# Kernel tuning notes

Measured on AMD Instinct MI355X. Metric: run time of the kernel, lower is better.

The kernel has to match this reference:

```python
import jax, jax.numpy as jnp
import numpy as np

NUM_HEADS = 12
H_PATCH = 14
W_PATCH = 14
ROPE_BASE = 10000.0


def _rope_2d(head_dim):
    # 2D RoPE: first half of head_dim encodes row (h), second half encodes col (w).
    half = head_dim // 2
    inv_freq = 1.0 / (ROPE_BASE ** (jnp.arange(0, half, 2, dtype=jnp.float32) / half))  # [half/2]
    ys = jnp.arange(H_PATCH)
    xs = jnp.arange(W_PATCH)
    yy, xx = jnp.meshgrid(ys, xs, indexing='ij')
    h_idx = yy.reshape(-1).astype(jnp.float32)  # [N]
    w_idx = xx.reshape(-1).astype(jnp.float32)  # [N]
    freqs_h = h_idx[:, None] * inv_freq[None, :]  # [N, half/2]
    freqs_w = w_idx[:, None] * inv_freq[None, :]  # [N, half/2]
    emb = jnp.concatenate([freqs_h, freqs_w], axis=-1)  # [N, half]
    emb = jnp.concatenate([emb, emb], axis=-1)          # [N, head_dim]
    return jnp.cos(emb), jnp.sin(emb)


def _rotate_half(x):
    d = x.shape[-1] // 2
    return jnp.concatenate([-x[..., d:], x[..., :d]], axis=-1)


def reference(x, qkv_w, qkv_b, proj_w, proj_b):
    BxT, N, C = x.shape
    hd = C // NUM_HEADS
    qkv = x @ qkv_w.T + qkv_b                                    # [BxT, N, 3C]
    qkv = qkv.reshape(BxT, N, 3, NUM_HEADS, hd)
    qkv = jnp.transpose(qkv, (2, 0, 3, 1, 4))                    # [3, BxT, H, N, hd]
    q, k, v = qkv[0], qkv[1], qkv[2]
    cos, sin = _rope_2d(hd)                                      # [N, hd]
    cos = cos[None, None, :, :]
    sin = sin[None, None, :, :]
    q = q * cos + _rotate_half(q) * sin
    k = k * cos + _rotate_half(k) * sin
    scale = hd ** -0.5
    attn = jnp.einsum('bhqd,bhkd->bhqk', q, k) * scale           # [BxT, H, N, N]
    attn = jax.nn.softmax(attn, axis=-1)
    out = jnp.einsum('bhqk,bhkd->bhqd', attn, v)                 # [BxT, H, N, hd]
    out = jnp.transpose(out, (0, 2, 1, 3)).reshape(BxT, N, C)
    out = out @ proj_w.T + proj_b
    return out


def setup_inputs() -> dict:
    key = jax.random.key(0)
    ks = jax.random.split(key, 5)
    C = 768
    return {
        'x': jax.random.normal(ks[0], (128, 196, C), dtype=jnp.float32),
        'qkv_w': jax.random.normal(ks[1], (3 * C, C), dtype=jnp.float32) * (C ** -0.5),
        'qkv_b': jax.random.normal(ks[2], (3 * C,), dtype=jnp.float32) * 0.02,
        'proj_w': jax.random.normal(ks[3], (C, C), dtype=jnp.float32) * (C ** -0.5),
        'proj_b': jax.random.normal(ks[4], (C,), dtype=jnp.float32) * 0.02,
    }
```

## Files before the change

### kernel.cpp

```cpp
#include <hip/hip_runtime.h>
#include <hip/hip_bf16.h>

typedef __attribute__((ext_vector_type(8))) short short8;
typedef __attribute__((ext_vector_type(4))) float f32x4;

#define GLD16(gp, lp) \
  __builtin_amdgcn_global_load_lds((const __attribute__((address_space(1))) void*)(gp), \
                                   (__attribute__((address_space(3))) void*)(lp), 16, 0, 0)

__device__ __forceinline__ f32x4 mfma_bf16(short8 a, short8 b, f32x4 c) {
  return __builtin_amdgcn_mfma_f32_16x16x32_bf16(a, b, c, 0, 0, 0);
}

__global__ __launch_bounds__(256) void cast_bf16_kernel(const float* __restrict__ src,
                                                        __hip_bfloat16* __restrict__ dst,
                                                        int n4) {
  int i = blockIdx.x * 256 + threadIdx.x;
  if (i >= n4) return;
  float4 v = reinterpret_cast<const float4*>(src)[i];
  ushort4 o;
  o.x = __builtin_bit_cast(unsigned short, __float2bfloat16(v.x));
  o.y = __builtin_bit_cast(unsigned short, __float2bfloat16(v.y));
  o.z = __builtin_bit_cast(unsigned short, __float2bfloat16(v.z));
  o.w = __builtin_bit_cast(unsigned short, __float2bfloat16(v.w));
  reinterpret_cast<ushort4*>(dst)[i] = o;
}

__global__ __launch_bounds__(256) void rope_table_kernel(float* __restrict__ cosT,
                                                         float* __restrict__ sinT) {
  int i = blockIdx.x * 256 + threadIdx.x;
  if (i >= 196 * 64) return;
  int t = i >> 6, d = i & 63;
  int c = d & 31;
  float pos = (c < 16) ? (float)(t / 14) : (float)(t % 14);
  int j = c & 15;
  float invf = expf(-(float)j * 0.5756462732485114f);
  float ang = pos * invf;
  cosT[i] = cosf(ang);
  sinT[i] = sinf(ang);
}

__global__ __launch_bounds__(256) void gemm_qkv_kernel(
    const __hip_bfloat16* __restrict__ A, const __hip_bfloat16* __restrict__ W,
    const float* __restrict__ bias, const float* __restrict__ cosT,
    const float* __restrict__ sinT, __hip_bfloat16* __restrict__ qb,
    __hip_bfloat16* __restrict__ kb, __hip_bfloat16* __restrict__ vb) {
  __shared__ __align__(16) __hip_bfloat16 As[128 * 64];
  __shared__ __align__(16) __hip_bfloat16 Bs[128 * 64];
  const int tid = threadIdx.x;
  const int id = blockIdx.x;
  const int sup = id / 72, rem = id % 72;
  const int bm = sup * 4 + rem / 18;
  const int bn = rem % 18;
  const int lane = tid & 63, wv = tid >> 6;
  const int wm = wv >> 1, wn = wv & 1;
  const int quad = lane >> 4, ln = lane & 15;

  const int r0 = tid >> 3;
  const int csw = ((tid & 7) ^ (r0 & 7)) * 8;
  const __hip_bfloat16* Ag = A + ((long)(bm * 128 + r0) * 768 + csw);
  const __hip_bfloat16* Wg = W + ((long)(bn * 128 + r0) * 768 + csw);
  __hip_bfloat16* As0 = As + tid * 8;
  __hip_bfloat16* Bs0 = Bs + tid * 8;

  const int c0 = (quad ^ (ln & 7)) * 8;
  const int c1 = c0 ^ 32;

  f32x4 acc[4][4];
#pragma unroll
  for (int i = 0; i < 4; i++)
#pragma unroll
    for (int j = 0; j < 4; j++) acc[i][j] = (f32x4){0.f, 0.f, 0.f, 0.f};

  for (int k0 = 0; k0 < 768; k0 += 64) {
    GLD16(Ag + k0,            As0);
    GLD16(Ag + 32 * 768 + k0, As0 + 2048);
    GLD16(Ag + 64 * 768 + k0, As0 + 4096);
    GLD16(Ag + 96 * 768 + k0, As0 + 6144);
    GLD16(Wg + k0,            Bs0);
    GLD16(Wg + 32 * 768 + k0, Bs0 + 2048);
    GLD16(Wg + 64 * 768 + k0, Bs0 + 4096);
    GLD16(Wg + 96 * 768 + k0, Bs0 + 6144);
    __syncthreads();
#pragma unroll
    for (int kk = 0; kk < 2; kk++) {
      const int cc = kk ? c1 : c0;
      short8 af[4], bf[4];
#pragma unroll
      for (int i = 0; i < 4; i++)
        af[i] = *(const short8*)(As + (wm * 64 + i * 16 + ln) * 64 + cc);
#pragma unroll
      for (int j = 0; j < 4; j++)
        bf[j] = *(const short8*)(Bs + (wn * 64 + j * 16 + ln) * 64 + cc);
#pragma unroll
      for (int i = 0; i < 4; i++)
#pragma unroll
        for (int j = 0; j < 4; j++) acc[i][j] = mfma_bf16(af[i], bf[j], acc[i][j]);
    }
    __syncthreads();
  }

  const int ncolbase = bn * 128 + wn * 64;
  const int s = ncolbase / 768;
  const int hh = (ncolbase % 768) >> 6;
  __hip_bfloat16* outb = (s == 0) ? qb : ((s == 1) ? kb : vb);
  float bi[4];
#pragma unroll
  for (int j = 0; j < 4; j++) bi[j] = bias[ncolbase + j * 16 + ln];
  const bool dorope = (s < 2);

#pragma unroll
  for (int i = 0; i < 4; i++) {
#pragma unroll
    for (int r = 0; r < 4; r++) {
      int m = bm * 128 + wm * 64 + i * 16 + quad * 4 + r;
      int b = m / 196, t = m - b * 196;
      float v0 = acc[i][0][r] + bi[0];
      float v1 = acc[i][1][r] + bi[1];
      float v2 = acc[i][2][r] + bi[2];
      float v3 = acc[i][3][r] + bi[3];
      if (dorope) {
        const float* ct = cosT + t * 64 + ln;
        const float* st = sinT + t * 64 + ln;
        float c0f = ct[0], c1f = ct[16], c2f = ct[32], c3f = ct[48];
        float s0 = st[0], s1 = st[16], s2 = st[32], s3 = st[48];
        float w0 = v0 * c0f - v2 * s0;
        float w1 = v1 * c1f - v3 * s1;
        float w2 = v2 * c2f + v0 * s2;
        float w3 = v3 * c3f + v1 * s3;
        v0 = w0; v1 = w1; v2 = w2; v3 = w3;
      }
      __hip_bfloat16* op = outb + ((long)(b * 12 + hh) * 196 + t) * 64 + ln;
      op[0]  = __float2bfloat16(v0);
      op[16] = __float2bfloat16(v1);
      op[32] = __float2bfloat16(v2);
      op[48] = __float2bfloat16(v3);
    }
  }
}

__global__ __launch_bounds__(256) void attn_kernel(
    const __hip_bfloat16* __restrict__ qb, const __hip_bfloat16* __restrict__ kb,
    const __hip_bfloat16* __restrict__ vb, __hip_bfloat16* __restrict__ att) {
  __shared__ __align__(16) __hip_bfloat16 Vt[64 * 232];
  __shared__ __align__(16) __hip_bfloat16 Ps[4][16 * 232];
  const int bh = blockIdx.x;
  const int b = bh / 12, h = bh - b * 12;
  const int tid = threadIdx.x;
  const int lane = tid & 63, wv = tid >> 6;
  const int quad = lane >> 4, ln = lane & 15;
  const __hip_bfloat16* qg = qb + (long)bh * (196 * 64);
  const __hip_bfloat16* kg = kb + (long)bh * (196 * 64);
  const __hip_bfloat16* vg = vb + (long)bh * (196 * 64);

  for (int ch = tid; ch < 224 * 8; ch += 256) {
    int row = ch >> 3, c = (ch & 7) * 8;
    unsigned short vals[8] = {0, 0, 0, 0, 0, 0, 0, 0};
    if (row < 196) *(uint4*)vals = *(const uint4*)(vg + row * 64 + c);
#pragma unroll
    for (int u = 0; u < 8; u++)
      ((unsigned short*)Vt)[(c + u) * 232 + row] = vals[u];
  }

  __hip_bfloat16* Pw = &Ps[wv][0];
#pragma unroll
  for (int r = 0; r < 4; r++)
    Pw[(quad * 4 + r) * 232 + 208 + ln] = __float2bfloat16(0.f);
  __syncthreads();

  for (int qt = wv; qt < 13; qt += 4) {
    int tok = qt * 16 + ln;
    if (tok > 195) tok = 195;
    short8 aq0 = *(const short8*)(qg + tok * 64 + quad * 8);
    short8 aq1 = *(const short8*)(qg + tok * 64 + 32 + quad * 8);

    f32x4 sacc[13];
#pragma unroll
    for (int ct = 0; ct < 13; ct++) {
      int krow = ct * 16 + ln;
      if (krow > 195) krow = 195;
      const __hip_bfloat16* kp = kg + krow * 64 + quad * 8;
      short8 b0 = *(const short8*)kp;
      short8 b1 = *(const short8*)(kp + 32);
      f32x4 cacc = (f32x4){0.f, 0.f, 0.f, 0.f};
      cacc = mfma_bf16(aq0, b0, cacc);
      cacc = mfma_bf16(aq1, b1, cacc);
      sacc[ct] = cacc;
    }

    float sm[4] = {0.f, 0.f, 0.f, 0.f};
#pragma unroll
    for (int ct = 0; ct < 13; ct++) {
      bool valid = (ct * 16 + ln) < 196;
#pragma unroll
      for (int r = 0; r < 4; r++) {
        float p = valid ? __expf(sacc[ct][r] * 0.125f) : 0.f;
        sm[r] += p;
        Pw[(quad * 4 + r) * 232 + ct * 16 + ln] = __float2bfloat16(p);
      }
    }
#pragma unroll
    for (int mk = 1; mk < 16; mk <<= 1) {
#pragma unroll
      for (int r = 0; r < 4; r++) sm[r] += __shfl_xor(sm[r], mk, 64);
    }
    asm volatile("" ::: "memory");

    f32x4 o[4];
#pragma unroll
    for (int j = 0; j < 4; j++) o[j] = (f32x4){0.f, 0.f, 0.f, 0.f};
#pragma unroll
    for (int kt = 0; kt < 7; kt++) {
      short8 pa = *(const short8*)(Pw + ln * 232 + kt * 32 + quad * 8);
#pragma unroll
      for (int j = 0; j < 4; j++) {
        short8 bv = *(const short8*)(Vt + (j * 16 + ln) * 232 + kt * 32 + quad * 8);
        o[j] = mfma_bf16(pa, bv, o[j]);
      }
    }
    asm volatile("" ::: "memory");

    float rl[4];
#pragma unroll
    for (int r = 0; r < 4; r++) rl[r] = 1.0f / sm[r];
    int trow = qt * 16 + quad * 4;
#pragma unroll
    for (int r = 0; r < 4; r++) {
      int t = trow + r;
      if (t < 196) {
        __hip_bfloat16* op = att + (long)(b * 196 + t) * 768 + h * 64 + ln;
#pragma unroll
        for (int j = 0; j < 4; j++) op[j * 16] = __float2bfloat16(o[j][r] * rl[r]);
      }
    }
  }
}

__global__ __launch_bounds__(256) void gemm_proj_kernel(
    const __hip_bfloat16* __restrict__ A, const __hip_bfloat16* __restrict__ W,
    const float* __restrict__ bias, float* __restrict__ out) {
  __shared__ __align__(16) __hip_bfloat16 As[128 * 64];
  __shared__ __align__(16) __hip_bfloat16 Bs[128 * 64];
  const int tid = threadIdx.x;
  const int id = blockIdx.x;
  const int sup = id / 24, rem = id % 24;
  const int bm = sup * 4 + rem / 6;
  const int bn = rem % 6;
  const int lane = tid & 63, wv = tid >> 6;
  const int wm = wv >> 1, wn = wv & 1;
  const int quad = lane >> 4, ln = lane & 15;

  const int r0 = tid >> 3;
  const int csw = ((tid & 7) ^ (r0 & 7)) * 8;
  const __hip_bfloat16* Ag = A + ((long)(bm * 128 + r0) * 768 + csw);
  const __hip_bfloat16* Wg = W + ((long)(bn * 128 + r0) * 768 + csw);
  __hip_bfloat16* As0 = As + tid * 8;
  __hip_bfloat16* Bs0 = Bs + tid * 8;

  const int c0 = (quad ^ (ln & 7)) * 8;
  const int c1 = c0 ^ 32;

  f32x4 acc[4][4];
#pragma unroll
  for (int i = 0; i < 4; i++)
#pragma unroll
    for (int j = 0; j < 4; j++) acc[i][j] = (f32x4){0.f, 0.f, 0.f, 0.f};

  for (int k0 = 0; k0 < 768; k0 += 64) {
    GLD16(Ag + k0,            As0);
    GLD16(Ag + 32 * 768 + k0, As0 + 2048);
    GLD16(Ag + 64 * 768 + k0, As0 + 4096);
    GLD16(Ag + 96 * 768 + k0, As0 + 6144);
    GLD16(Wg + k0,            Bs0);
    GLD16(Wg + 32 * 768 + k0, Bs0 + 2048);
    GLD16(Wg + 64 * 768 + k0, Bs0 + 4096);
    GLD16(Wg + 96 * 768 + k0, Bs0 + 6144);
    __syncthreads();
#pragma unroll
    for (int kk = 0; kk < 2; kk++) {
      const int cc = kk ? c1 : c0;
      short8 af[4], bf[4];
#pragma unroll
      for (int i = 0; i < 4; i++)
        af[i] = *(const short8*)(As + (wm * 64 + i * 16 + ln) * 64 + cc);
#pragma unroll
      for (int j = 0; j < 4; j++)
        bf[j] = *(const short8*)(Bs + (wn * 64 + j * 16 + ln) * 64 + cc);
#pragma unroll
      for (int i = 0; i < 4; i++)
#pragma unroll
        for (int j = 0; j < 4; j++) acc[i][j] = mfma_bf16(af[i], bf[j], acc[i][j]);
    }
    __syncthreads();
  }

  const int ncolbase = bn * 128 + wn * 64;
  float bi[4];
#pragma unroll
  for (int j = 0; j < 4; j++) bi[j] = bias[ncolbase + j * 16 + ln];
#pragma unroll
  for (int i = 0; i < 4; i++) {
#pragma unroll
    for (int r = 0; r < 4; r++) {
      int m = bm * 128 + wm * 64 + i * 16 + quad * 4 + r;
      float* op = out + (long)m * 768 + ncolbase + ln;
      op[0]  = acc[i][0][r] + bi[0];
      op[16] = acc[i][1][r] + bi[1];
      op[32] = acc[i][2][r] + bi[2];
      op[48] = acc[i][3][r] + bi[3];
    }
  }
}

extern "C" void kernel_launch(void* const* d_in, const int* in_sizes, int n_in,
                              void* d_out, int out_size, void* d_ws, size_t ws_size,
                              hipStream_t stream) {
  const float* x      = (const float*)d_in[0];
  const float* qkv_w  = (const float*)d_in[1];
  const float* qkv_b  = (const float*)d_in[2];
  const float* proj_w = (const float*)d_in[3];
  const float* proj_b = (const float*)d_in[4];
  float* out = (float*)d_out;
  (void)in_sizes; (void)n_in; (void)out_size; (void)ws_size;

  char* ws = (char*)d_ws;
  size_t off = 0;
  auto alloc = [&](size_t bytes) -> void* {
    void* p = (void*)(ws + off);
    off += (bytes + 255) & ~(size_t)255;
    return p;
  };
  const size_t MB0 = (size_t)25088 * 768 * 2;
  __hip_bfloat16* xb   = (__hip_bfloat16*)alloc(MB0);
  __hip_bfloat16* w1b  = (__hip_bfloat16*)alloc((size_t)2304 * 768 * 2);
  __hip_bfloat16* w2b  = (__hip_bfloat16*)alloc((size_t)768 * 768 * 2);
  float* cosT          = (float*)alloc(196 * 64 * 4);
  float* sinT          = (float*)alloc(196 * 64 * 4);
  __hip_bfloat16* qbuf = (__hip_bfloat16*)alloc(MB0);
  __hip_bfloat16* kbuf = (__hip_bfloat16*)alloc(MB0);
  __hip_bfloat16* vbuf = (__hip_bfloat16*)alloc(MB0);
  __hip_bfloat16* attb = xb;

  cast_bf16_kernel<<<18816, 256, 0, stream>>>(x, xb, 25088 * 768 / 4);
  cast_bf16_kernel<<<1728, 256, 0, stream>>>(qkv_w, w1b, 2304 * 768 / 4);
  cast_bf16_kernel<<<576, 256, 0, stream>>>(proj_w, w2b, 768 * 768 / 4);
  rope_table_kernel<<<49, 256, 0, stream>>>(cosT, sinT);
  gemm_qkv_kernel<<<3528, 256, 0, stream>>>(xb, w1b, qkv_b, cosT, sinT,
                                            qbuf, kbuf, vbuf);
  attn_kernel<<<1536, 256, 0, stream>>>(qbuf, kbuf, vbuf, attb);
  gemm_proj_kernel<<<1176, 256, 0, stream>>>(attb, w2b, proj_b, out);
}
```

Baseline: 378.0 us.

## Widen GEMM N-tiles to 256 and merge cast/rope prep into one kernel

Both GEMMs move from 128x128 to 128x256 block tiles, so each wave computes a 64x128 sub-tile with a 4x8 MFMA accumulator array. This halves the grid and raises reuse of A fragments per LDS load. It also drops the grouped (super-block) rasterization in favour of a plain row-major order. The three cast launches and the rope-table launch are folded into a single prep kernel to cut launch overhead. In exchange, the larger tiles double the accumulator registers and B-tile LDS, which lowers occupancy, and the proj GEMM now launches only 588 blocks.

```diff
diff --git a/kernel.cpp b/kernel.cpp
--- a/kernel.cpp
+++ b/kernel.cpp
@@ -12,32 +12,42 @@
   return __builtin_amdgcn_mfma_f32_16x16x32_bf16(a, b, c, 0, 0, 0);
 }
 
-__global__ __launch_bounds__(256) void cast_bf16_kernel(const float* __restrict__ src,
-                                                        __hip_bfloat16* __restrict__ dst,
-                                                        int n4) {
+__global__ __launch_bounds__(256) void prep_kernel(
+    const float* __restrict__ x, const float* __restrict__ w1,
+    const float* __restrict__ w2, __hip_bfloat16* __restrict__ xb,
+    __hip_bfloat16* __restrict__ w1b, __hip_bfloat16* __restrict__ w2b,
+    float* __restrict__ cosT, float* __restrict__ sinT) {
+  const int N1 = 4816896;
+  const int N2 = N1 + 442368;
+  const int N3 = N2 + 147456;
   int i = blockIdx.x * 256 + threadIdx.x;
-  if (i >= n4) return;
-  float4 v = reinterpret_cast<const float4*>(src)[i];
-  ushort4 o;
-  o.x = __builtin_bit_cast(unsigned short, __float2bfloat16(v.x));
-  o.y = __builtin_bit_cast(unsigned short, __float2bfloat16(v.y));
-  o.z = __builtin_bit_cast(unsigned short, __float2bfloat16(v.z));
-  o.w = __builtin_bit_cast(unsigned short, __float2bfloat16(v.w));
-  reinterpret_cast<ushort4*>(dst)[i] = o;
-}
-
-__global__ __launch_bounds__(256) void rope_table_kernel(float* __restrict__ cosT,
-                                                         float* __restrict__ sinT) {
-  int i = blockIdx.x * 256 + threadIdx.x;
-  if (i >= 196 * 64) return;
-  int t = i >> 6, d = i & 63;
-  int c = d & 31;
-  float pos = (c < 16) ? (float)(t / 14) : (float)(t % 14);
-  int j = c & 15;
-  float invf = expf(-(float)j * 0.5756462732485114f);
-  float ang = pos * invf;
-  cosT[i] = cosf(ang);
-  sinT[i] = sinf(ang);
+  if (i < N3) {
+    const float* src;
+    __hip_bfloat16* dst;
+    int j;
+    if (i < N1) { src = x; dst = xb; j = i; }
+    else if (i < N2) { src = w1; dst = w1b; j = i - N1; }
+    else { src = w2; dst = w2b; j = i - N2; }
+    float4 v = reinterpret_cast<const float4*>(src)[j];
+    ushort4 o;
+    o.x = __builtin_bit_cast(unsigned short, __float2bfloat16(v.x));
+    o.y = __builtin_bit_cast(unsigned short, __float2bfloat16(v.y));
+    o.z = __builtin_bit_cast(unsigned short, __float2bfloat16(v.z));
+    o.w = __builtin_bit_cast(unsigned short, __float2bfloat16(v.w));
+    reinterpret_cast<ushort4*>(dst)[j] = o;
+  } else {
+    int r = i - N3;
+    if (r < 196 * 64) {
+      int t = r >> 6, d = r & 63;
+      int c = d & 31;
+      float pos = (c < 16) ? (float)(t / 14) : (float)(t % 14);
+      int jj = c & 15;
+      float invf = expf(-(float)jj * 0.5756462732485114f);
+      float ang = pos * invf;
+      cosT[r] = cosf(ang);
+      sinT[r] = sinf(ang);
+    }
+  }
 }
 
 __global__ __launch_bounds__(256) void gemm_qkv_kernel(
@@ -46,12 +56,10 @@
     const float* __restrict__ sinT, __hip_bfloat16* __restrict__ qb,
     __hip_bfloat16* __restrict__ kb, __hip_bfloat16* __restrict__ vb) {
   __shared__ __align__(16) __hip_bfloat16 As[128 * 64];
-  __shared__ __align__(16) __hip_bfloat16 Bs[128 * 64];
+  __shared__ __align__(16) __hip_bfloat16 Bs[256 * 64];
   const int tid = threadIdx.x;
   const int id = blockIdx.x;
-  const int sup = id / 72, rem = id % 72;
-  const int bm = sup * 4 + rem / 18;
-  const int bn = rem % 18;
+  const int bm = id / 9, bn = id % 9;
   const int lane = tid & 63, wv = tid >> 6;
   const int wm = wv >> 1, wn = wv & 1;
   const int quad = lane >> 4, ln = lane & 15;
@@ -59,54 +67,50 @@
   const int r0 = tid >> 3;
   const int csw = ((tid & 7) ^ (r0 & 7)) * 8;
   const __hip_bfloat16* Ag = A + ((long)(bm * 128 + r0) * 768 + csw);
-  const __hip_bfloat16* Wg = W + ((long)(bn * 128 + r0) * 768 + csw);
+  const __hip_bfloat16* Wg = W + ((long)(bn * 256 + r0) * 768 + csw);
   __hip_bfloat16* As0 = As + tid * 8;
   __hip_bfloat16* Bs0 = Bs + tid * 8;
 
   const int c0 = (quad ^ (ln & 7)) * 8;
   const int c1 = c0 ^ 32;
 
-  f32x4 acc[4][4];
+  f32x4 acc[4][8];
 #pragma unroll
   for (int i = 0; i < 4; i++)
 #pragma unroll
-    for (int j = 0; j < 4; j++) acc[i][j] = (f32x4){0.f, 0.f, 0.f, 0.f};
+    for (int j = 0; j < 8; j++) acc[i][j] = (f32x4){0.f, 0.f, 0.f, 0.f};
 
   for (int k0 = 0; k0 < 768; k0 += 64) {
-    GLD16(Ag + k0,            As0);
-    GLD16(Ag + 32 * 768 + k0, As0 + 2048);
-    GLD16(Ag + 64 * 768 + k0, As0 + 4096);
-    GLD16(Ag + 96 * 768 + k0, As0 + 6144);
-    GLD16(Wg + k0,            Bs0);
-    GLD16(Wg + 32 * 768 + k0, Bs0 + 2048);
-    GLD16(Wg + 64 * 768 + k0, Bs0 + 4096);
-    GLD16(Wg + 96 * 768 + k0, Bs0 + 6144);
+#pragma unroll
+    for (int b = 0; b < 4; b++) GLD16(Ag + (long)b * 32 * 768 + k0, As0 + b * 2048);
+#pragma unroll
+    for (int b = 0; b < 8; b++) GLD16(Wg + (long)b * 32 * 768 + k0, Bs0 + b * 2048);
     __syncthreads();
 #pragma unroll
     for (int kk = 0; kk < 2; kk++) {
       const int cc = kk ? c1 : c0;
-      short8 af[4], bf[4];
+      short8 af[4], bf[8];
 #pragma unroll
       for (int i = 0; i < 4; i++)
         af[i] = *(const short8*)(As + (wm * 64 + i * 16 + ln) * 64 + cc);
 #pragma unroll
-      for (int j = 0; j < 4; j++)
-        bf[j] = *(const short8*)(Bs + (wn * 64 + j * 16 + ln) * 64 + cc);
+      for (int j = 0; j < 8; j++)
+        bf[j] = *(const short8*)(Bs + (wn * 128 + j * 16 + ln) * 64 + cc);
 #pragma unroll
       for (int i = 0; i < 4; i++)
 #pragma unroll
-        for (int j = 0; j < 4; j++) acc[i][j] = mfma_bf16(af[i], bf[j], acc[i][j]);
+        for (int j = 0; j < 8; j++) acc[i][j] = mfma_bf16(af[i], bf[j], acc[i][j]);
     }
     __syncthreads();
   }
 
-  const int ncolbase = bn * 128 + wn * 64;
-  const int s = ncolbase / 768;
-  const int hh = (ncolbase % 768) >> 6;
+  const int ncb = bn * 256 + wn * 128;
+  const int s = ncb / 768;
+  const int h0 = (ncb % 768) >> 6;
   __hip_bfloat16* outb = (s == 0) ? qb : ((s == 1) ? kb : vb);
-  float bi[4];
-#pragma unroll
-  for (int j = 0; j < 4; j++) bi[j] = bias[ncolbase + j * 16 + ln];
+  float bi[8];
+#pragma unroll
+  for (int j = 0; j < 8; j++) bi[j] = bias[ncb + j * 16 + ln];
   const bool dorope = (s < 2);
 
 #pragma unroll
@@ -115,26 +119,31 @@
     for (int r = 0; r < 4; r++) {
       int m = bm * 128 + wm * 64 + i * 16 + quad * 4 + r;
       int b = m / 196, t = m - b * 196;
-      float v0 = acc[i][0][r] + bi[0];
-      float v1 = acc[i][1][r] + bi[1];
-      float v2 = acc[i][2][r] + bi[2];
-      float v3 = acc[i][3][r] + bi[3];
+      float v[8];
+#pragma unroll
+      for (int j = 0; j < 8; j++) v[j] = acc[i][j][r] + bi[j];
       if (dorope) {
         const float* ct = cosT + t * 64 + ln;
         const float* st = sinT + t * 64 + ln;
-        float c0f = ct[0], c1f = ct[16], c2f = ct[32], c3f = ct[48];
-        float s0 = st[0], s1 = st[16], s2 = st[32], s3 = st[48];
-        float w0 = v0 * c0f - v2 * s0;
-        float w1 = v1 * c1f - v3 * s1;
-        float w2 = v2 * c2f + v0 * s2;
-        float w3 = v3 * c3f + v1 * s3;
-        v0 = w0; v1 = w1; v2 = w2; v3 = w3;
+        float cv[4], sv[4];
+#pragma unroll
+        for (int u = 0; u < 4; u++) { cv[u] = ct[u * 16]; sv[u] = st[u * 16]; }
+#pragma unroll
+        for (int p = 0; p < 4; p++) {
+          int jl = (p & 1) + (p & 2) * 2;
+          int jh = jl + 2;
+          int dl = jl & 3, dh = dl + 2;
+          float lo = v[jl] * cv[dl] - v[jh] * sv[dl];
+          float hi = v[jh] * cv[dh] + v[jl] * sv[dh];
+          v[jl] = lo; v[jh] = hi;
+        }
       }
-      __hip_bfloat16* op = outb + ((long)(b * 12 + hh) * 196 + t) * 64 + ln;
-      op[0]  = __float2bfloat16(v0);
-      op[16] = __float2bfloat16(v1);
-      op[32] = __float2bfloat16(v2);
-      op[48] = __float2bfloat16(v3);
+      __hip_bfloat16* op0 = outb + ((long)(b * 12 + h0) * 196 + t) * 64 + ln;
+      __hip_bfloat16* op1 = op0 + 196 * 64;
+#pragma unroll
+      for (int j = 0; j < 4; j++) op0[j * 16] = __float2bfloat16(v[j]);
+#pragma unroll
+      for (int j = 0; j < 4; j++) op1[j * 16] = __float2bfloat16(v[4 + j]);
     }
   }
 }
@@ -240,12 +249,10 @@
     const __hip_bfloat16* __restrict__ A, const __hip_bfloat16* __restrict__ W,
     const float* __restrict__ bias, float* __restrict__ out) {
   __shared__ __align__(16) __hip_bfloat16 As[128 * 64];
-  __shared__ __align__(16) __hip_bfloat16 Bs[128 * 64];
+  __shared__ __align__(16) __hip_bfloat16 Bs[256 * 64];
   const int tid = threadIdx.x;
   const int id = blockIdx.x;
-  const int sup = id / 24, rem = id % 24;
-  const int bm = sup * 4 + rem / 6;
-  const int bn = rem % 6;
+  const int bm = id / 3, bn = id % 3;
   const int lane = tid & 63, wv = tid >> 6;
   const int wm = wv >> 1, wn = wv & 1;
   const int quad = lane >> 4, ln = lane & 15;
@@ -253,61 +260,55 @@
   const int r0 = tid >> 3;
   const int csw = ((tid & 7) ^ (r0 & 7)) * 8;
   const __hip_bfloat16* Ag = A + ((long)(bm * 128 + r0) * 768 + csw);
-  const __hip_bfloat16* Wg = W + ((long)(bn * 128 + r0) * 768 + csw);
+  const __hip_bfloat16* Wg = W + ((long)(bn * 256 + r0) * 768 + csw);
   __hip_bfloat16* As0 = As + tid * 8;
   __hip_bfloat16* Bs0 = Bs + tid * 8;
 
   const int c0 = (quad ^ (ln & 7)) * 8;
   const int c1 = c0 ^ 32;
 
-  f32x4 acc[4][4];
+  f32x4 acc[4][8];
 #pragma unroll
   for (int i = 0; i < 4; i++)
 #pragma unroll
-    for (int j = 0; j < 4; j++) acc[i][j] = (f32x4){0.f, 0.f, 0.f, 0.f};
+    for (int j = 0; j < 8; j++) acc[i][j] = (f32x4){0.f, 0.f, 0.f, 0.f};
 
   for (int k0 = 0; k0 < 768; k0 += 64) {
-    GLD16(Ag + k0,            As0);
-    GLD16(Ag + 32 * 768 + k0, As0 + 2048);
-    GLD16(Ag + 64 * 768 + k0, As0 + 4096);
-    GLD16(Ag + 96 * 768 + k0, As0 + 6144);
-    GLD16(Wg + k0,            Bs0);
-    GLD16(Wg + 32 * 768 + k0, Bs0 + 2048);
-    GLD16(Wg + 64 * 768 + k0, Bs0 + 4096);
-    GLD16(Wg + 96 * 768 + k0, Bs0 + 6144);
+#pragma unroll
+    for (int b = 0; b < 4; b++) GLD16(Ag + (long)b * 32 * 768 + k0, As0 + b * 2048);
+#pragma unroll
+    for (int b = 0; b < 8; b++) GLD16(Wg + (long)b * 32 * 768 + k0, Bs0 + b * 2048);
     __syncthreads();
 #pragma unroll
     for (int kk = 0; kk < 2; kk++) {
       const int cc = kk ? c1 : c0;
-      short8 af[4], bf[4];
+      short8 af[4], bf[8];
 #pragma unroll
       for (int i = 0; i < 4; i++)
         af[i] = *(const short8*)(As + (wm * 64 + i * 16 + ln) * 64 + cc);
 #pragma unroll
-      for (int j = 0; j < 4; j++)
-        bf[j] = *(const short8*)(Bs + (wn * 64 + j * 16 + ln) * 64 + cc);
+      for (int j = 0; j < 8; j++)
+        bf[j] = *(const short8*)(Bs + (wn * 128 + j * 16 + ln) * 64 + cc);
 #pragma unroll
       for (int i = 0; i < 4; i++)
 #pragma unroll
-        for (int j = 0; j < 4; j++) acc[i][j] = mfma_bf16(af[i], bf[j], acc[i][j]);
+        for (int j = 0; j < 8; j++) acc[i][j] = mfma_bf16(af[i], bf[j], acc[i][j]);
     }
     __syncthreads();
   }
 
-  const int ncolbase = bn * 128 + wn * 64;
-  float bi[4];
-#pragma unroll
-  for (int j = 0; j < 4; j++) bi[j] = bias[ncolbase + j * 16 + ln];
+  const int ncb = bn * 256 + wn * 128;
+  float bi[8];
+#pragma unroll
+  for (int j = 0; j < 8; j++) bi[j] = bias[ncb + j * 16 + ln];
 #pragma unroll
   for (int i = 0; i < 4; i++) {
 #pragma unroll
     for (int r = 0; r < 4; r++) {
       int m = bm * 128 + wm * 64 + i * 16 + quad * 4 + r;
-      float* op = out + (long)m * 768 + ncolbase + ln;
-      op[0]  = acc[i][0][r] + bi[0];
-      op[16] = acc[i][1][r] + bi[1];
-      op[32] = acc[i][2][r] + bi[2];
-      op[48] = acc[i][3][r] + bi[3];
+      float* op = out + (long)m * 768 + ncb + ln;
+#pragma unroll
+      for (int j = 0; j < 8; j++) op[j * 16] = acc[i][j][r] + bi[j];
     }
   }
 }
@@ -341,12 +342,9 @@
   __hip_bfloat16* vbuf = (__hip_bfloat16*)alloc(MB0);
   __hip_bfloat16* attb = xb;
 
-  cast_bf16_kernel<<<18816, 256, 0, stream>>>(x, xb, 25088 * 768 / 4);
-  cast_bf16_kernel<<<1728, 256, 0, stream>>>(qkv_w, w1b, 2304 * 768 / 4);
-  cast_bf16_kernel<<<576, 256, 0, stream>>>(proj_w, w2b, 768 * 768 / 4);
-  rope_table_kernel<<<49, 256, 0, stream>>>(cosT, sinT);
-  gemm_qkv_kernel<<<3528, 256, 0, stream>>>(xb, w1b, qkv_b, cosT, sinT,
+  prep_kernel<<<21169, 256, 0, stream>>>(x, qkv_w, proj_w, xb, w1b, w2b, cosT, sinT);
+  gemm_qkv_kernel<<<1764, 256, 0, stream>>>(xb, w1b, qkv_b, cosT, sinT,
                                             qbuf, kbuf, vbuf);
   attn_kernel<<<1536, 256, 0, stream>>>(qbuf, kbuf, vbuf, attb);
-  gemm_proj_kernel<<<1176, 256, 0, stream>>>(attb, w2b, proj_b, out);
-}
+  gemm_proj_kernel<<<588, 256, 0, stream>>>(attb, w2b, proj_b, out);
+}
```

Measured after the change: 454.3 us. 1.2x slower.
